# Kernel optimization log

Measured on AMD Instinct MI355X. Metric: run time of the kernel, lower is better.

Reference implementation:

```python
import jax, jax.numpy as jnp
import numpy as np

B, S, CV, CT = 256, 257, 1024, 768
EPS_LN = 1e-5
NEG_SLOPE = 0.01

def _layernorm(x, g, b):
    mu = jnp.mean(x, axis=-1, keepdims=True)
    var = jnp.mean(jnp.square(x - mu), axis=-1, keepdims=True)
    return (x - mu) * jax.lax.rsqrt(var + EPS_LN) * g + b

def _leaky(x):
    return jnp.where(x >= 0, x, NEG_SLOPE * x)

def setup_inputs() -> dict:
    key = jax.random.key(0)
    ks = jax.random.split(key, 12)
    d = {
        "vis_hidden": jax.random.normal(ks[0], (B, S, CV), jnp.float32),
        "inf_hidden": jax.random.normal(ks[1], (B, S, CV), jnp.float32),
        "topk": 3,
        "W0": jax.random.normal(ks[2], (2 * CV, CV), jnp.float32) * 0.02,
        "b0": jnp.zeros((CV,), jnp.float32),
        "g0": jnp.ones((CV,), jnp.float32),
        "be0": jnp.zeros((CV,), jnp.float32),
        "W1": jax.random.normal(ks[3], (CV, CV), jnp.float32) * 0.02,
        "b1": jnp.zeros((CV,), jnp.float32),
        "g1": jnp.ones((CV,), jnp.float32),
        "be1": jnp.zeros((CV,), jnp.float32),
        "W2": jax.random.normal(ks[4], (CV, CV), jnp.float32) * 0.02,
        "b2": jnp.zeros((CV,), jnp.float32),
        "g2": jnp.ones((CV,), jnp.float32),
        "be2": jnp.zeros((CV,), jnp.float32),
        "W3": jax.random.normal(ks[5], (CV, CT), jnp.float32) * 0.02,
        "b3": jnp.zeros((CT,), jnp.float32),
    }
    return d

def reference(vis_hidden, inf_hidden, topk, W0, b0, g0, be0, W1, b1, g1, be1,
              W2, b2, g2, be2, W3, b3):
    vis_tok = vis_hidden[:, 1:, :]   # [B, N, C]
    inf_tok = inf_hidden[:, 1:, :]
    vis_n = vis_tok / jnp.linalg.norm(vis_tok, axis=-1, keepdims=True)
    inf_n = inf_tok / jnp.linalg.norm(inf_tok, axis=-1, keepdims=True)
    cos_sim = jnp.sum(vis_n * inf_n, axis=-1)          # [B, N]
    _, idx = jax.lax.top_k(cos_sim, topk)              # [B, k]
    idx3 = idx[:, :, None]                              # [B, k, 1]
    vis_k = jnp.take_along_axis(vis_tok, idx3, axis=1)  # [B, k, C]
    inf_k = jnp.take_along_axis(inf_tok, idx3, axis=1)
    vis_k = jnp.concatenate([vis_k, vis_hidden[:, 0:1, :]], axis=1)  # [B, k+1, C]
    inf_k = jnp.concatenate([inf_k, inf_hidden[:, 0:1, :]], axis=1)
    x = jnp.concatenate([vis_k, inf_k], axis=-1)        # [B, k+1, 2C]
    x = _leaky(_layernorm(x @ W0 + b0, g0, be0))
    x = _leaky(_layernorm(x @ W1 + b1, g1, be1))
    x = _leaky(_layernorm(x @ W2 + b2, g2, be2))
    return x @ W3 + b3                                   # [B, k+1, CT]
```

## Files before the change

### kernel.cpp

```cpp
#include <hip/hip_runtime.h>
#include <math.h>

#define BB 256
#define SS 257
#define CVD 1024
#define CTD 768
#define NTOK 256
#define MROWS 1024
#define EPS_LN 1e-5f
#define NEG_SLOPE 0.01f
#define LDKP 72

typedef __bf16 bf16x8 __attribute__((ext_vector_type(8)));
typedef float f32x4 __attribute__((ext_vector_type(4)));
typedef unsigned short usx8 __attribute__((ext_vector_type(8)));
typedef unsigned short usx4 __attribute__((ext_vector_type(4)));

__device__ __forceinline__ unsigned short f2bf(float x) {
    unsigned u = __float_as_uint(x);
    unsigned r = u + 0x7FFFu + ((u >> 16) & 1u);
    return (unsigned short)(r >> 16);
}
__device__ __forceinline__ float bf2f(unsigned short h) {
    return __uint_as_float(((unsigned)h) << 16);
}
__device__ __forceinline__ void cvt4(float a, float b, float c, float d, usx4& h, usx4& l) {
    h[0] = f2bf(a); l[0] = f2bf(a - bf2f(h[0]));
    h[1] = f2bf(b); l[1] = f2bf(b - bf2f(h[1]));
    h[2] = f2bf(c); l[2] = f2bf(c - bf2f(h[2]));
    h[3] = f2bf(d); l[3] = f2bf(d - bf2f(h[3]));
}

__global__ __launch_bounds__(256) void cos_kernel(const float* __restrict__ vis,
                                                  const float* __restrict__ inf,
                                                  float* __restrict__ cosv) {
    int wave = threadIdx.x >> 6;
    int lane = threadIdx.x & 63;
    int r = blockIdx.x * 4 + wave;
    int b = r >> 8, s = r & 255;
    const float4* vrow = (const float4*)(vis + (size_t)b * SS * CVD + (size_t)(s + 1) * CVD);
    const float4* irow = (const float4*)(inf + (size_t)b * SS * CVD + (size_t)(s + 1) * CVD);
    float vv = 0.f, ii = 0.f, vi = 0.f;
#pragma unroll
    for (int j = 0; j < 4; ++j) {
        float4 v = vrow[j * 64 + lane];
        float4 w = irow[j * 64 + lane];
        vv += v.x * v.x + v.y * v.y + v.z * v.z + v.w * v.w;
        ii += w.x * w.x + w.y * w.y + w.z * w.z + w.w * w.w;
        vi += v.x * w.x + v.y * w.y + v.z * w.z + v.w * w.w;
    }
#pragma unroll
    for (int off = 32; off; off >>= 1) {
        vv += __shfl_xor(vv, off);
        ii += __shfl_xor(ii, off);
        vi += __shfl_xor(vi, off);
    }
    if (lane == 0) cosv[r] = vi / sqrtf(vv * ii);
}

__global__ __launch_bounds__(64) void topk_kernel(const float* __restrict__ cosv,
                                                  int* __restrict__ idx) {
    int b = blockIdx.x;
    int lane = threadIdx.x;
    float v[4];
    int id[4];
#pragma unroll
    for (int j = 0; j < 4; ++j) {
        id[j] = lane + j * 64;
        v[j] = cosv[b * NTOK + id[j]];
    }
    for (int round = 0; round < 3; ++round) {
        float bv = v[0];
        int bi = id[0];
#pragma unroll
        for (int j = 1; j < 4; ++j)
            if (v[j] > bv) { bv = v[j]; bi = id[j]; }
#pragma unroll
        for (int off = 32; off; off >>= 1) {
            float ov = __shfl_xor(bv, off);
            int oi = __shfl_xor(bi, off);
            if (ov > bv || (ov == bv && oi < bi)) { bv = ov; bi = oi; }
        }
        if (lane == 0) idx[b * 3 + round] = bi;
#pragma unroll
        for (int j = 0; j < 4; ++j)
            if (id[j] == bi) v[j] = -3.402823466e38f;
    }
}

__global__ __launch_bounds__(256) void gather_conv_kernel(const float* __restrict__ vis,
                                                          const float* __restrict__ inf,
                                                          const int* __restrict__ idx,
                                                          unsigned short* __restrict__ x0h,
                                                          unsigned short* __restrict__ x0l) {
    int r = blockIdx.x, t = threadIdx.x;
    int b = r >> 2, j = r & 3;
    int tok = (j < 3) ? (idx[b * 3 + j] + 1) : 0;
    const float4* v = (const float4*)(vis + (size_t)b * SS * CVD + (size_t)tok * CVD);
    const float4* w = (const float4*)(inf + (size_t)b * SS * CVD + (size_t)tok * CVD);
    float4 a = v[t];
    float4 c = w[t];
    usx4 h, l;
    cvt4(a.x, a.y, a.z, a.w, h, l);
    *(usx4*)(x0h + (size_t)r * 2048 + t * 4) = h;
    *(usx4*)(x0l + (size_t)r * 2048 + t * 4) = l;
    cvt4(c.x, c.y, c.z, c.w, h, l);
    *(usx4*)(x0h + (size_t)r * 2048 + 1024 + t * 4) = h;
    *(usx4*)(x0l + (size_t)r * 2048 + 1024 + t * 4) = l;
}

__global__ __launch_bounds__(256) void wprep_kernel(const float* __restrict__ W,
                                                    unsigned short* __restrict__ WTh,
                                                    unsigned short* __restrict__ WTl,
                                                    int K, int N) {
    __shared__ float tile[64][69];
    int k0 = blockIdx.x * 64, n0 = blockIdx.y * 64;
    int t = threadIdx.x;
    int r = t >> 4, c4 = (t & 15) * 4;
#pragma unroll
    for (int p = 0; p < 4; ++p) {
        float4 v = *(const float4*)(W + (size_t)(k0 + r + p * 16) * N + n0 + c4);
        tile[r + p * 16][c4 + 0] = v.x;
        tile[r + p * 16][c4 + 1] = v.y;
        tile[r + p * 16][c4 + 2] = v.z;
        tile[r + p * 16][c4 + 3] = v.w;
    }
    __syncthreads();
    int nn0 = t >> 4, kk = (t & 15) * 4;
#pragma unroll
    for (int p = 0; p < 4; ++p) {
        int nn = nn0 + p * 16;
        float a = tile[kk + 0][nn], b = tile[kk + 1][nn];
        float c = tile[kk + 2][nn], d = tile[kk + 3][nn];
        usx4 h, l;
        cvt4(a, b, c, d, h, l);
        *(usx4*)(WTh + (size_t)(n0 + nn) * K + k0 + kk) = h;
        *(usx4*)(WTl + (size_t)(n0 + nn) * K + k0 + kk) = l;
    }
}

__global__ __launch_bounds__(256, 1) void gemm_split_kernel(
        const unsigned short* __restrict__ Ah, const unsigned short* __restrict__ Al,
        const unsigned short* __restrict__ Bh, const unsigned short* __restrict__ Bl,
        float* __restrict__ Cpart, int N, int K, int KCH) {
    __shared__ unsigned short sAh[128 * LDKP], sAl[128 * LDKP];
    __shared__ unsigned short sBh[128 * LDKP], sBl[128 * LDKP];
    int t = threadIdx.x;
    int lane = t & 63, wid = t >> 6;
    int wm = (wid >> 1) * 64, wn = (wid & 1) * 64;
    int fr = lane & 15, kg = lane >> 4;
    int m0 = blockIdx.y * 128, n0 = blockIdx.x * 128;
    int kstart = blockIdx.z * KCH;
    int sm = t >> 1, skq = (t & 1) * 32;
    const usx8* gAh = (const usx8*)(Ah + (size_t)(m0 + sm) * K + kstart + skq);
    const usx8* gAl = (const usx8*)(Al + (size_t)(m0 + sm) * K + kstart + skq);
    const usx8* gBh = (const usx8*)(Bh + (size_t)(n0 + sm) * K + kstart + skq);
    const usx8* gBl = (const usx8*)(Bl + (size_t)(n0 + sm) * K + kstart + skq);

    f32x4 acc[4][4] = {};
    usx8 rah[4], ral[4], rbh[4], rbl[4];
    int nsteps = KCH >> 6;

#pragma unroll
    for (int s = 0; s < 4; ++s) { rah[s] = gAh[s]; ral[s] = gAl[s]; rbh[s] = gBh[s]; rbl[s] = gBl[s]; }

    for (int step = 0; step < nsteps; ++step) {
        int base = sm * LDKP + skq;
#pragma unroll
        for (int s = 0; s < 4; ++s) {
            *(usx8*)&sAh[base + s * 8] = rah[s];
            *(usx8*)&sAl[base + s * 8] = ral[s];
            *(usx8*)&sBh[base + s * 8] = rbh[s];
            *(usx8*)&sBl[base + s * 8] = rbl[s];
        }
        __syncthreads();
        if (step + 1 < nsteps) {
            int adv = (step + 1) * 8;
#pragma unroll
            for (int s = 0; s < 4; ++s) {
                rah[s] = gAh[adv + s]; ral[s] = gAl[adv + s];
                rbh[s] = gBh[adv + s]; rbl[s] = gBl[adv + s];
            }
        }
#pragma unroll
        for (int kc = 0; kc < 2; ++kc) {
            int kb = kc * 32 + kg * 8;
            bf16x8 ah[4], al[4];
#pragma unroll
            for (int i = 0; i < 4; ++i) {
                int ro = (wm + i * 16 + fr) * LDKP + kb;
                ah[i] = *(const bf16x8*)&sAh[ro];
                al[i] = *(const bf16x8*)&sAl[ro];
            }
#pragma unroll
            for (int j = 0; j < 4; ++j) {
                int co = (wn + j * 16 + fr) * LDKP + kb;
                bf16x8 bh = *(const bf16x8*)&sBh[co];
                bf16x8 bl = *(const bf16x8*)&sBl[co];
#pragma unroll
                for (int i = 0; i < 4; ++i) {
                    acc[i][j] = __builtin_amdgcn_mfma_f32_16x16x32_bf16(ah[i], bh, acc[i][j], 0, 0, 0);
                    acc[i][j] = __builtin_amdgcn_mfma_f32_16x16x32_bf16(ah[i], bl, acc[i][j], 0, 0, 0);
                    acc[i][j] = __builtin_amdgcn_mfma_f32_16x16x32_bf16(al[i], bh, acc[i][j], 0, 0, 0);
                }
            }
        }
        __syncthreads();
    }
    float* Cp = Cpart + (size_t)blockIdx.z * MROWS * N;
#pragma unroll
    for (int i = 0; i < 4; ++i) {
#pragma unroll
        for (int j = 0; j < 4; ++j) {
            int row = m0 + wm + i * 16 + kg * 4;
            int col = n0 + wn + j * 16 + fr;
#pragma unroll
            for (int r = 0; r < 4; ++r)
                Cp[(size_t)(row + r) * N + col] = acc[i][j][r];
        }
    }
}

__device__ __forceinline__ float block_sum(float x, float* red) {
#pragma unroll
    for (int off = 32; off; off >>= 1) x += __shfl_xor(x, off);
    int wave = threadIdx.x >> 6, lane = threadIdx.x & 63;
    if (lane == 0) red[wave] = x;
    __syncthreads();
    float r = red[0] + red[1] + red[2] + red[3];
    __syncthreads();
    return r;
}

__global__ __launch_bounds__(256) void reduce_ln_kernel(const float* __restrict__ Cp,
                                                        const float* __restrict__ bias,
                                                        const float* __restrict__ g,
                                                        const float* __restrict__ be,
                                                        unsigned short* __restrict__ Xh,
                                                        unsigned short* __restrict__ Xl) {
    __shared__ float red[4];
    int row = blockIdx.x, t = threadIdx.x;
    float4 y0 = ((const float4*)(Cp + (size_t)row * CVD))[t];
    float4 y1 = ((const float4*)(Cp + 1048576 + (size_t)row * CVD))[t];
    float4 y2 = ((const float4*)(Cp + 2097152 + (size_t)row * CVD))[t];
    float4 y3 = ((const float4*)(Cp + 3145728 + (size_t)row * CVD))[t];
    float4 bv = ((const float4*)bias)[t];
    float vx = y0.x + y1.x + y2.x + y3.x + bv.x;
    float vy = y0.y + y1.y + y2.y + y3.y + bv.y;
    float vz = y0.z + y1.z + y2.z + y3.z + bv.z;
    float vw = y0.w + y1.w + y2.w + y3.w + bv.w;
    float tot = block_sum(vx + vy + vz + vw, red);
    float mu = tot * (1.0f / CVD);
    float dx = vx - mu, dy = vy - mu, dz = vz - mu, dw = vw - mu;
    float tot2 = block_sum(dx * dx + dy * dy + dz * dz + dw * dw, red);
    float rstd = rsqrtf(tot2 * (1.0f / CVD) + EPS_LN);
    float4 gg = ((const float4*)g)[t];
    float4 bb = ((const float4*)be)[t];
    float ox = dx * rstd * gg.x + bb.x;
    float oy = dy * rstd * gg.y + bb.y;
    float oz = dz * rstd * gg.z + bb.z;
    float ow = dw * rstd * gg.w + bb.w;
    ox = ox >= 0.f ? ox : NEG_SLOPE * ox;
    oy = oy >= 0.f ? oy : NEG_SLOPE * oy;
    oz = oz >= 0.f ? oz : NEG_SLOPE * oz;
    ow = ow >= 0.f ? ow : NEG_SLOPE * ow;
    usx4 h, l;
    cvt4(ox, oy, oz, ow, h, l);
    *(usx4*)(Xh + (size_t)row * CVD + t * 4) = h;
    *(usx4*)(Xl + (size_t)row * CVD + t * 4) = l;
}

__global__ __launch_bounds__(192) void reduce_out_kernel(const float* __restrict__ Cp,
                                                         const float* __restrict__ bias,
                                                         float* __restrict__ out) {
    int row = blockIdx.x, t = threadIdx.x;
    float4 y0 = ((const float4*)(Cp + (size_t)row * CTD))[t];
    float4 y1 = ((const float4*)(Cp + 786432 + (size_t)row * CTD))[t];
    float4 y2 = ((const float4*)(Cp + 1572864 + (size_t)row * CTD))[t];
    float4 y3 = ((const float4*)(Cp + 2359296 + (size_t)row * CTD))[t];
    float4 bv = ((const float4*)bias)[t];
    float4 o;
    o.x = y0.x + y1.x + y2.x + y3.x + bv.x;
    o.y = y0.y + y1.y + y2.y + y3.y + bv.y;
    o.z = y0.z + y1.z + y2.z + y3.z + bv.z;
    o.w = y0.w + y1.w + y2.w + y3.w + bv.w;
    ((float4*)(out + (size_t)row * CTD))[t] = o;
}

extern "C" void kernel_launch(void* const* d_in, const int* in_sizes, int n_in,
                              void* d_out, int out_size, void* d_ws, size_t ws_size,
                              hipStream_t stream) {
    const float* vis = (const float*)d_in[0];
    const float* inf = (const float*)d_in[1];
    const float* W0 = (const float*)d_in[3];
    const float* b0 = (const float*)d_in[4];
    const float* g0 = (const float*)d_in[5];
    const float* be0 = (const float*)d_in[6];
    const float* W1 = (const float*)d_in[7];
    const float* b1 = (const float*)d_in[8];
    const float* g1 = (const float*)d_in[9];
    const float* be1 = (const float*)d_in[10];
    const float* W2 = (const float*)d_in[11];
    const float* b2 = (const float*)d_in[12];
    const float* g2 = (const float*)d_in[13];
    const float* be2 = (const float*)d_in[14];
    const float* W3 = (const float*)d_in[15];
    const float* b3 = (const float*)d_in[16];
    float* out = (float*)d_out;

    char* ws = (char*)d_ws;
    float* cosv = (float*)(ws + 0x0);
    int* idx = (int*)(ws + 0x40000);
    unsigned short* x0h = (unsigned short*)(ws + 0x50000);
    unsigned short* x0l = (unsigned short*)(ws + 0x450000);
    unsigned short* Xh = (unsigned short*)(ws + 0x850000);
    unsigned short* Xl = (unsigned short*)(ws + 0xA50000);
    unsigned short* W0h = (unsigned short*)(ws + 0xC50000);
    unsigned short* W0l = (unsigned short*)(ws + 0x1050000);
    unsigned short* W1h = (unsigned short*)(ws + 0x1450000);
    unsigned short* W1l = (unsigned short*)(ws + 0x1650000);
    unsigned short* W2h = (unsigned short*)(ws + 0x1850000);
    unsigned short* W2l = (unsigned short*)(ws + 0x1A50000);
    unsigned short* W3h = (unsigned short*)(ws + 0x1C50000);
    unsigned short* W3l = (unsigned short*)(ws + 0x1DD0000);
    float* Cpart = (float*)(ws + 0x1F50000);

    cos_kernel<<<dim3(16384), dim3(256), 0, stream>>>(vis, inf, cosv);
    topk_kernel<<<dim3(BB), dim3(64), 0, stream>>>(cosv, idx);
    gather_conv_kernel<<<dim3(MROWS), dim3(256), 0, stream>>>(vis, inf, idx, x0h, x0l);

    wprep_kernel<<<dim3(32, 16), dim3(256), 0, stream>>>(W0, W0h, W0l, 2048, 1024);
    wprep_kernel<<<dim3(16, 16), dim3(256), 0, stream>>>(W1, W1h, W1l, 1024, 1024);
    wprep_kernel<<<dim3(16, 16), dim3(256), 0, stream>>>(W2, W2h, W2l, 1024, 1024);
    wprep_kernel<<<dim3(16, 12), dim3(256), 0, stream>>>(W3, W3h, W3l, 1024, 768);

    gemm_split_kernel<<<dim3(8, 8, 4), dim3(256), 0, stream>>>(x0h, x0l, W0h, W0l, Cpart, 1024, 2048, 512);
    reduce_ln_kernel<<<dim3(MROWS), dim3(256), 0, stream>>>(Cpart, b0, g0, be0, Xh, Xl);

    gemm_split_kernel<<<dim3(8, 8, 4), dim3(256), 0, stream>>>(Xh, Xl, W1h, W1l, Cpart, 1024, 1024, 256);
    reduce_ln_kernel<<<dim3(MROWS), dim3(256), 0, stream>>>(Cpart, b1, g1, be1, Xh, Xl);

    gemm_split_kernel<<<dim3(8, 8, 4), dim3(256), 0, stream>>>(Xh, Xl, W2h, W2l, Cpart, 1024, 1024, 256);
    reduce_ln_kernel<<<dim3(MROWS), dim3(256), 0, stream>>>(Cpart, b2, g2, be2, Xh, Xl);

    gemm_split_kernel<<<dim3(6, 8, 4), dim3(256), 0, stream>>>(Xh, Xl, W3h, W3l, Cpart, 768, 1024, 256);
    reduce_out_kernel<<<dim3(MROWS), dim3(192), 0, stream>>>(Cpart, b3, out);
}
```

Before: 652.0 us.

## Fuse cosine, top-k and gather into one per-batch kernel; merge weight prep launches

```diff
diff --git a/kernel.cpp b/kernel.cpp
--- a/kernel.cpp
+++ b/kernel.cpp
@@ -31,90 +31,121 @@
     h[3] = f2bf(d); l[3] = f2bf(d - bf2f(h[3]));
 }
 
-__global__ __launch_bounds__(256) void cos_kernel(const float* __restrict__ vis,
-                                                  const float* __restrict__ inf,
-                                                  float* __restrict__ cosv) {
-    int wave = threadIdx.x >> 6;
-    int lane = threadIdx.x & 63;
-    int r = blockIdx.x * 4 + wave;
-    int b = r >> 8, s = r & 255;
-    const float4* vrow = (const float4*)(vis + (size_t)b * SS * CVD + (size_t)(s + 1) * CVD);
-    const float4* irow = (const float4*)(inf + (size_t)b * SS * CVD + (size_t)(s + 1) * CVD);
-    float vv = 0.f, ii = 0.f, vi = 0.f;
-#pragma unroll
-    for (int j = 0; j < 4; ++j) {
-        float4 v = vrow[j * 64 + lane];
-        float4 w = irow[j * 64 + lane];
-        vv += v.x * v.x + v.y * v.y + v.z * v.z + v.w * v.w;
-        ii += w.x * w.x + w.y * w.y + w.z * w.z + w.w * w.w;
-        vi += v.x * w.x + v.y * w.y + v.z * w.z + v.w * w.w;
-    }
-#pragma unroll
-    for (int off = 32; off; off >>= 1) {
-        vv += __shfl_xor(vv, off);
-        ii += __shfl_xor(ii, off);
-        vi += __shfl_xor(vi, off);
-    }
-    if (lane == 0) cosv[r] = vi / sqrtf(vv * ii);
-}
-
-__global__ __launch_bounds__(64) void topk_kernel(const float* __restrict__ cosv,
-                                                  int* __restrict__ idx) {
+__global__ __launch_bounds__(512) void front_kernel(const float* __restrict__ vis,
+                                                    const float* __restrict__ inf,
+                                                    unsigned short* __restrict__ x0h,
+                                                    unsigned short* __restrict__ x0l) {
+    __shared__ float cosv[NTOK];
+    __shared__ int sidx[3];
     int b = blockIdx.x;
-    int lane = threadIdx.x;
-    float v[4];
-    int id[4];
-#pragma unroll
-    for (int j = 0; j < 4; ++j) {
-        id[j] = lane + j * 64;
-        v[j] = cosv[b * NTOK + id[j]];
-    }
-    for (int round = 0; round < 3; ++round) {
-        float bv = v[0];
-        int bi = id[0];
-#pragma unroll
-        for (int j = 1; j < 4; ++j)
-            if (v[j] > bv) { bv = v[j]; bi = id[j]; }
+    int t = threadIdx.x;
+    int wave = t >> 6, lane = t & 63;
+    const float* vbase = vis + (size_t)b * SS * CVD;
+    const float* ibase = inf + (size_t)b * SS * CVD;
+
+    for (int u = 0; u < 16; ++u) {
+        int r0 = wave * 32 + u * 2;
+        const float4* v0 = (const float4*)(vbase + (size_t)(r0 + 1) * CVD);
+        const float4* i0 = (const float4*)(ibase + (size_t)(r0 + 1) * CVD);
+        const float4* v1 = (const float4*)(vbase + (size_t)(r0 + 2) * CVD);
+        const float4* i1 = (const float4*)(ibase + (size_t)(r0 + 2) * CVD);
+        float vv0 = 0.f, ii0 = 0.f, vi0 = 0.f;
+        float vv1 = 0.f, ii1 = 0.f, vi1 = 0.f;
+#pragma unroll
+        for (int j = 0; j < 4; ++j) {
+            float4 a = v0[j * 64 + lane];
+            float4 c = i0[j * 64 + lane];
+            float4 d = v1[j * 64 + lane];
+            float4 e = i1[j * 64 + lane];
+            vv0 += a.x * a.x + a.y * a.y + a.z * a.z + a.w * a.w;
+            ii0 += c.x * c.x + c.y * c.y + c.z * c.z + c.w * c.w;
+            vi0 += a.x * c.x + a.y * c.y + a.z * c.z + a.w * c.w;
+            vv1 += d.x * d.x + d.y * d.y + d.z * d.z + d.w * d.w;
+            ii1 += e.x * e.x + e.y * e.y + e.z * e.z + e.w * e.w;
+            vi1 += d.x * e.x + d.y * e.y + d.z * e.z + d.w * e.w;
+        }
 #pragma unroll
         for (int off = 32; off; off >>= 1) {
-            float ov = __shfl_xor(bv, off);
-            int oi = __shfl_xor(bi, off);
-            if (ov > bv || (ov == bv && oi < bi)) { bv = ov; bi = oi; }
-        }
-        if (lane == 0) idx[b * 3 + round] = bi;
-#pragma unroll
-        for (int j = 0; j < 4; ++j)
-            if (id[j] == bi) v[j] = -3.402823466e38f;
-    }
-}
-
-__global__ __launch_bounds__(256) void gather_conv_kernel(const float* __restrict__ vis,
-                                                          const float* __restrict__ inf,
-                                                          const int* __restrict__ idx,
-                                                          unsigned short* __restrict__ x0h,
-                                                          unsigned short* __restrict__ x0l) {
-    int r = blockIdx.x, t = threadIdx.x;
-    int b = r >> 2, j = r & 3;
-    int tok = (j < 3) ? (idx[b * 3 + j] + 1) : 0;
-    const float4* v = (const float4*)(vis + (size_t)b * SS * CVD + (size_t)tok * CVD);
-    const float4* w = (const float4*)(inf + (size_t)b * SS * CVD + (size_t)tok * CVD);
-    float4 a = v[t];
-    float4 c = w[t];
-    usx4 h, l;
-    cvt4(a.x, a.y, a.z, a.w, h, l);
-    *(usx4*)(x0h + (size_t)r * 2048 + t * 4) = h;
-    *(usx4*)(x0l + (size_t)r * 2048 + t * 4) = l;
-    cvt4(c.x, c.y, c.z, c.w, h, l);
-    *(usx4*)(x0h + (size_t)r * 2048 + 1024 + t * 4) = h;
-    *(usx4*)(x0l + (size_t)r * 2048 + 1024 + t * 4) = l;
-}
-
-__global__ __launch_bounds__(256) void wprep_kernel(const float* __restrict__ W,
-                                                    unsigned short* __restrict__ WTh,
-                                                    unsigned short* __restrict__ WTl,
-                                                    int K, int N) {
+            vv0 += __shfl_xor(vv0, off);
+            ii0 += __shfl_xor(ii0, off);
+            vi0 += __shfl_xor(vi0, off);
+            vv1 += __shfl_xor(vv1, off);
+            ii1 += __shfl_xor(ii1, off);
+            vi1 += __shfl_xor(vi1, off);
+        }
+        if (lane == 0) {
+            cosv[r0] = vi0 / sqrtf(vv0 * ii0);
+            cosv[r0 + 1] = vi1 / sqrtf(vv1 * ii1);
+        }
+    }
+    __syncthreads();
+
+    if (wave == 0) {
+        float v[4];
+        int id[4];
+#pragma unroll
+        for (int j = 0; j < 4; ++j) {
+            id[j] = lane + j * 64;
+            v[j] = cosv[id[j]];
+        }
+        for (int round = 0; round < 3; ++round) {
+            float bv = v[0];
+            int bi = id[0];
+#pragma unroll
+            for (int j = 1; j < 4; ++j)
+                if (v[j] > bv) { bv = v[j]; bi = id[j]; }
+#pragma unroll
+            for (int off = 32; off; off >>= 1) {
+                float ov = __shfl_xor(bv, off);
+                int oi = __shfl_xor(bi, off);
+                if (ov > bv || (ov == bv && oi < bi)) { bv = ov; bi = oi; }
+            }
+            if (lane == 0) sidx[round] = bi;
+#pragma unroll
+            for (int j = 0; j < 4; ++j)
+                if (id[j] == bi) v[j] = -3.402823466e38f;
+        }
+    }
+    __syncthreads();
+
+    int c = t & 255;
+    int half = (t >> 8);
+    const float* src_base = half ? ibase : vbase;
+#pragma unroll
+    for (int rr = 0; rr < 4; ++rr) {
+        int tok = (rr < 3) ? (sidx[rr] + 1) : 0;
+        float4 a = ((const float4*)(src_base + (size_t)tok * CVD))[c];
+        usx4 h, l;
+        cvt4(a.x, a.y, a.z, a.w, h, l);
+        size_t off = (size_t)(b * 4 + rr) * 2048 + half * 1024 + c * 4;
+        *(usx4*)(x0h + off) = h;
+        *(usx4*)(x0l + off) = l;
+    }
+}
+
+__global__ __launch_bounds__(256) void wprep_all_kernel(
+        const float* __restrict__ W0, unsigned short* __restrict__ W0h, unsigned short* __restrict__ W0l,
+        const float* __restrict__ W1, unsigned short* __restrict__ W1h, unsigned short* __restrict__ W1l,
+        const float* __restrict__ W2, unsigned short* __restrict__ W2h, unsigned short* __restrict__ W2l,
+        const float* __restrict__ W3, unsigned short* __restrict__ W3h, unsigned short* __restrict__ W3l) {
     __shared__ float tile[64][69];
-    int k0 = blockIdx.x * 64, n0 = blockIdx.y * 64;
+    int bid = blockIdx.x;
+    const float* W;
+    unsigned short *Th, *Tl;
+    int K, N, k0, n0;
+    if (bid < 512) {
+        int q = bid;       W = W0; Th = W0h; Tl = W0l; K = 2048; N = 1024;
+        k0 = (q & 31) * 64; n0 = (q >> 5) * 64;
+    } else if (bid < 768) {
+        int q = bid - 512; W = W1; Th = W1h; Tl = W1l; K = 1024; N = 1024;
+        k0 = (q & 15) * 64; n0 = (q >> 4) * 64;
+    } else if (bid < 1024) {
+        int q = bid - 768; W = W2; Th = W2h; Tl = W2l; K = 1024; N = 1024;
+        k0 = (q & 15) * 64; n0 = (q >> 4) * 64;
+    } else {
+        int q = bid - 1024; W = W3; Th = W3h; Tl = W3l; K = 1024; N = 768;
+        k0 = (q & 15) * 64; n0 = (q >> 4) * 64;
+    }
     int t = threadIdx.x;
     int r = t >> 4, c4 = (t & 15) * 4;
 #pragma unroll
@@ -134,8 +165,8 @@
         float c = tile[kk + 2][nn], d = tile[kk + 3][nn];
         usx4 h, l;
         cvt4(a, b, c, d, h, l);
-        *(usx4*)(WTh + (size_t)(n0 + nn) * K + k0 + kk) = h;
-        *(usx4*)(WTl + (size_t)(n0 + nn) * K + k0 + kk) = l;
+        *(usx4*)(Th + (size_t)(n0 + nn) * K + k0 + kk) = h;
+        *(usx4*)(Tl + (size_t)(n0 + nn) * K + k0 + kk) = l;
     }
 }
 
@@ -309,8 +340,6 @@
     float* out = (float*)d_out;
 
     char* ws = (char*)d_ws;
-    float* cosv = (float*)(ws + 0x0);
-    int* idx = (int*)(ws + 0x40000);
     unsigned short* x0h = (unsigned short*)(ws + 0x50000);
     unsigned short* x0l = (unsigned short*)(ws + 0x450000);
     unsigned short* Xh = (unsigned short*)(ws + 0x850000);
@@ -325,14 +354,9 @@
     unsigned short* W3l = (unsigned short*)(ws + 0x1DD0000);
     float* Cpart = (float*)(ws + 0x1F50000);
 
-    cos_kernel<<<dim3(16384), dim3(256), 0, stream>>>(vis, inf, cosv);
-    topk_kernel<<<dim3(BB), dim3(64), 0, stream>>>(cosv, idx);
-    gather_conv_kernel<<<dim3(MROWS), dim3(256), 0, stream>>>(vis, inf, idx, x0h, x0l);
-
-    wprep_kernel<<<dim3(32, 16), dim3(256), 0, stream>>>(W0, W0h, W0l, 2048, 1024);
-    wprep_kernel<<<dim3(16, 16), dim3(256), 0, stream>>>(W1, W1h, W1l, 1024, 1024);
-    wprep_kernel<<<dim3(16, 16), dim3(256), 0, stream>>>(W2, W2h, W2l, 1024, 1024);
-    wprep_kernel<<<dim3(16, 12), dim3(256), 0, stream>>>(W3, W3h, W3l, 1024, 768);
+    front_kernel<<<dim3(BB), dim3(512), 0, stream>>>(vis, inf, x0h, x0l);
+    wprep_all_kernel<<<dim3(1216), dim3(256), 0, stream>>>(W0, W0h, W0l, W1, W1h, W1l,
+                                                           W2, W2h, W2l, W3, W3h, W3l);
 
     gemm_split_kernel<<<dim3(8, 8, 4), dim3(256), 0, stream>>>(x0h, x0l, W0h, W0l, Cpart, 1024, 2048, 512);
     reduce_ln_kernel<<<dim3(MROWS), dim3(256), 0, stream>>>(Cpart, b0, g0, be0, Xh, Xl);
```

Result: slower. 665.5 us (+2.1%).
